# Performance work log

Hardware: AMD Instinct MI355X
Metric: run time of the kernel (lower is better)

The kernel has to match this reference:

```python
import jax, jax.numpy as jnp
import numpy as np

B, T, I, H, O = 8192, 1024, 2, 10, 2


def _gru_scan(gates_x, W_hh, b_hh, collect):
    """gates_x: [B,T,3H] precomputed input-side gates. Returns outputs [B,T,H] if collect else final h [B,H]."""
    def step(h, gx):
        gh = h @ W_hh.T + b_hh                      # [B,3H]
        xr, xz, xn = jnp.split(gx, 3, axis=-1)
        hr, hz, hn = jnp.split(gh, 3, axis=-1)
        r = jax.nn.sigmoid(xr + hr)
        z = jax.nn.sigmoid(xz + hz)
        n = jnp.tanh(xn + r * hn)
        h_new = (1.0 - z) * n + z * h
        return h_new, (h_new if collect else None)
    h0 = jnp.zeros((gates_x.shape[0], W_hh.shape[1]), gates_x.dtype)
    hT, ys = jax.lax.scan(step, h0, jnp.swapaxes(gates_x, 0, 1))  # scan over time
    return jnp.swapaxes(ys, 0, 1) if collect else hT


def setup_inputs() -> dict:
    key = jax.random.key(0)
    ks = jax.random.split(key, 12)
    s = 1.0 / np.sqrt(H)  # PyTorch GRU/Linear init scale
    u = lambda k, shp: jax.random.uniform(k, shp, jnp.float32, -s, s)
    return {
        "batchX": jax.random.normal(ks[0], (B, T, I), jnp.float32),
        "W_ih0": u(ks[1], (3 * H, I)),  "W_hh0": u(ks[2], (3 * H, H)),
        "b_ih0": u(ks[3], (3 * H,)),    "b_hh0": u(ks[4], (3 * H,)),
        "W_ih1": u(ks[5], (3 * H, H)),  "W_hh1": u(ks[6], (3 * H, H)),
        "b_ih1": u(ks[7], (3 * H,)),    "b_hh1": u(ks[8], (3 * H,)),
        "W_fc": u(ks[9], (O, H)),       "b_fc": u(ks[10], (O,)),
    }


def reference(batchX, W_ih0, W_hh0, b_ih0, b_hh0, W_ih1, W_hh1, b_ih1, b_hh1, W_fc, b_fc):
    # Layer 0: need full sequence of hidden states (feeds layer 1)
    gx0 = batchX @ W_ih0.T + b_ih0                  # [B,T,3H] one big GEMM
    h1 = _gru_scan(gx0, W_hh0, b_hh0, collect=True)  # [B,T,H]
    # Layer 1: only final hidden state is used by the head
    gx1 = h1 @ W_ih1.T + b_ih1                      # [B,T,3H]
    hT = _gru_scan(gx1, W_hh1, b_hh1, collect=False)  # [B,H]
    return hT @ W_fc.T + b_fc                       # [B,O]
```

## Files before the change

### kernel.cpp

```cpp
#include <hip/hip_runtime.h>

#define NB 8192
#define NT 1024
#define NH 10
#define ROWS_PER_WAVE 4
#define ROWS_PER_BLOCK 16

typedef float v2f __attribute__((ext_vector_type(2)));
typedef float v4f __attribute__((ext_vector_type(4)));

#define LOG2E 1.44269504088896340736f

__device__ __forceinline__ float rcpf(float x) { return __builtin_amdgcn_rcpf(x); }
__device__ __forceinline__ float exp2i(float x) {
#if __has_builtin(__builtin_amdgcn_exp2f)
    return __builtin_amdgcn_exp2f(x);
#else
    float r;
    asm("v_exp_f32 %0, %1" : "=v"(r) : "v"(x));
    return r;
#endif
}
__device__ __forceinline__ float tanh2u(float u) { return fmaf(-2.0f, rcpf(exp2i(u) + 1.0f), 1.0f); }
__device__ __forceinline__ void sigm2q2(float qa, float qb, float& sa, float& sb) {
    const float da = 1.0f + exp2i(qa);
    const float db = 1.0f + exp2i(qb);
    const float R = rcpf(da * db);
    sa = db * R;
    sb = da * R;
}

__device__ __forceinline__ v2f lo2(v4f a) { return __builtin_shufflevector(a, a, 0, 1); }
__device__ __forceinline__ v2f hi2(v4f a) { return __builtin_shufflevector(a, a, 2, 3); }
__device__ __forceinline__ v2f pkfma(v2f a, v2f b, v2f c) {
    return __builtin_elementwise_fma(a, b, c);
}

struct W5 { v2f p[5]; };
__device__ __forceinline__ W5 loadrow_scaled(const float* __restrict__ q, float s) {
    W5 w;
#pragma unroll
    for (int k = 0; k < 5; ++k) w.p[k] = (v2f){q[2 * k] * s, q[2 * k + 1] * s};
    return w;
}
__device__ __forceinline__ v2f dotWacc(const W5& w, v4f ha, v4f hb, v2f hc, v2f acc) {
    acc = pkfma(w.p[0], lo2(ha), acc);
    acc = pkfma(w.p[1], hi2(ha), acc);
    acc = pkfma(w.p[2], lo2(hb), acc);
    acc = pkfma(w.p[3], hi2(hb), acc);
    acc = pkfma(w.p[4], hc, acc);
    return acc;
}
__device__ __forceinline__ float hsum(v2f a) { return a.x + a.y; }

__global__ __launch_bounds__(256) void gru_fused(
    const float* __restrict__ X,
    const float* __restrict__ Wih0, const float* __restrict__ Whh0,
    const float* __restrict__ bih0, const float* __restrict__ bhh0,
    const float* __restrict__ Wih1, const float* __restrict__ Whh1,
    const float* __restrict__ bih1, const float* __restrict__ bhh1,
    const float* __restrict__ Wfc,  const float* __restrict__ bfc,
    float* __restrict__ out)
{
    __shared__ __align__(16) float hls[4][2][5][12];

    const int tid  = threadIdx.x;
    const int lane = tid & 63;
    const int wave = tid >> 6;
    const int g    = lane / 10;
    const int j    = lane - g * 10;
    const int gg   = (g < 4) ? g : 4;

    const bool active = (g < ROWS_PER_WAVE);
    int b = blockIdx.x * ROWS_PER_BLOCK + wave * ROWS_PER_WAVE + (active ? g : 0);
    const bool store_ok = active && (b < NB);
    if (b >= NB) b = NB - 1;

    const int r0 = j, r1 = j + 10, r2 = j + 20;
    const float Sz = -LOG2E;
    const float Sn = 2.0f * LOG2E;

    const v2f wxr = (v2f){Wih0[r0 * 2] * Sz, Wih0[r0 * 2 + 1] * Sz};
    const v2f wxz = (v2f){Wih0[r1 * 2] * Sz, Wih0[r1 * 2 + 1] * Sz};
    const v2f wxn = (v2f){Wih0[r2 * 2] * Sn, Wih0[r2 * 2 + 1] * Sn};

    const W5 whr0 = loadrow_scaled(Whh0 + r0 * NH, Sz);
    const W5 whz0 = loadrow_scaled(Whh0 + r1 * NH, Sz);
    const W5 whn0 = loadrow_scaled(Whh0 + r2 * NH, Sn);
    const W5 wir1 = loadrow_scaled(Wih1 + r0 * NH, Sz);
    const W5 wiz1 = loadrow_scaled(Wih1 + r1 * NH, Sz);
    const W5 win1 = loadrow_scaled(Wih1 + r2 * NH, Sn);
    const W5 whr1 = loadrow_scaled(Whh1 + r0 * NH, Sz);
    const W5 whz1 = loadrow_scaled(Whh1 + r1 * NH, Sz);
    const W5 whn1 = loadrow_scaled(Whh1 + r2 * NH, Sn);

    const v2f sr0 = (v2f){(bih0[r0] + bhh0[r0]) * Sz, 0.0f};
    const v2f sz0 = (v2f){(bih0[r1] + bhh0[r1]) * Sz, 0.0f};
    const v2f sx0 = (v2f){bih0[r2] * Sn, 0.0f};
    const v2f sh0 = (v2f){bhh0[r2] * Sn, 0.0f};
    const v2f sr1 = (v2f){(bih1[r0] + bhh1[r0]) * Sz, 0.0f};
    const v2f sz1 = (v2f){(bih1[r1] + bhh1[r1]) * Sz, 0.0f};
    const v2f sx1 = (v2f){bih1[r2] * Sn, 0.0f};
    const v2f sh1 = (v2f){bhh1[r2] * Sn, 0.0f};

    float* const L0 = &hls[wave][0][gg][0];
    float* const L1 = &hls[wave][1][gg][0];

    v4f h0a = (v4f){0,0,0,0}, h0b = (v4f){0,0,0,0}; v2f h0c = (v2f){0,0};
    v4f h1a, h1b; v2f h1c;
    v4f nh1a = (v4f){0,0,0,0}, nh1b = (v4f){0,0,0,0}; v2f nh1c = (v2f){0,0};
    float my0 = 0.0f, my1 = 0.0f;

    const float2* xp = reinterpret_cast<const float2*>(X) + (size_t)b * NT;
    float2 xc = xp[0];
    float2 xn2;

    v2f accr, accz, accx, acch, aqr, aqz, aqx, aqh;
    v4f nh0a, nh0b; v2f nh0c;
    float r0v, z0v, n0v, r1v, z1v, n1v;

#define L0_GATES(xv)                                                            \
    accr = pkfma(wxr, xv, sr0);                                                 \
    accz = pkfma(wxz, xv, sz0);                                                 \
    accx = pkfma(wxn, xv, sx0);                                                 \
    accr = dotWacc(whr0, h0a, h0b, h0c, accr);                                  \
    accz = dotWacc(whz0, h0a, h0b, h0c, accz);                                  \
    acch = dotWacc(whn0, h0a, h0b, h0c, sh0);                                   \
    sigm2q2(hsum(accr), hsum(accz), r0v, z0v);                                  \
    n0v = tanh2u(fmaf(r0v, hsum(acch), hsum(accx)));                            \
    my0 = fmaf(z0v, my0 - n0v, n0v);                                            \
    L0[j] = my0;                                                                \
    nh0a = *reinterpret_cast<const v4f*>(L0);                                   \
    nh0b = *reinterpret_cast<const v4f*>(L0 + 4);                               \
    nh0c = *reinterpret_cast<const v2f*>(L0 + 8)

#define L1_GATES()                                                              \
    aqr = dotWacc(whr1, h1a, h1b, h1c, sr1);                                    \
    aqz = dotWacc(whz1, h1a, h1b, h1c, sz1);                                    \
    aqh = dotWacc(whn1, h1a, h1b, h1c, sh1);                                    \
    aqr = dotWacc(wir1, h0a, h0b, h0c, aqr);                                    \
    aqz = dotWacc(wiz1, h0a, h0b, h0c, aqz);                                    \
    aqx = dotWacc(win1, h0a, h0b, h0c, sx1);                                    \
    sigm2q2(hsum(aqr), hsum(aqz), r1v, z1v);                                    \
    n1v = tanh2u(fmaf(r1v, hsum(aqh), hsum(aqx)));                              \
    my1 = fmaf(z1v, my1 - n1v, n1v)

    {
        const v2f xv = (v2f){xc.x, xc.y};
        L0_GATES(xv);
        h0a = nh0a; h0b = nh0b; h0c = nh0c;
        xc = xp[1];
    }

    for (int t = 1; t < NT; ++t) {
        xn2 = xp[(t + 1 < NT) ? (t + 1) : (NT - 1)];
        const v2f xv = (v2f){xc.x, xc.y};
        L0_GATES(xv);
        h1a = nh1a; h1b = nh1b; h1c = nh1c;
        L1_GATES();
        h0a = nh0a; h0b = nh0b; h0c = nh0c;
        L1[j] = my1;
        nh1a = *reinterpret_cast<const v4f*>(L1);
        nh1b = *reinterpret_cast<const v4f*>(L1 + 4);
        nh1c = *reinterpret_cast<const v2f*>(L1 + 8);
        xc = xn2;
    }

    {
        h1a = nh1a; h1b = nh1b; h1c = nh1c;
        L1_GATES();
        L1[j] = my1;
        h1a = *reinterpret_cast<const v4f*>(L1);
        h1b = *reinterpret_cast<const v4f*>(L1 + 4);
        h1c = *reinterpret_cast<const v2f*>(L1 + 8);
    }
#undef L0_GATES
#undef L1_GATES

    if (store_ok && j < 2) {
        const W5 wf = loadrow_scaled(Wfc + j * NH, 1.0f);
        out[(size_t)b * 2 + j] = hsum(dotWacc(wf, h1a, h1b, h1c, (v2f){bfc[j], 0.0f}));
    }
}

extern "C" void kernel_launch(void* const* d_in, const int* in_sizes, int n_in,
                              void* d_out, int out_size, void* d_ws, size_t ws_size,
                              hipStream_t stream) {
    const float* X    = (const float*)d_in[0];
    const float* Wih0 = (const float*)d_in[1];
    const float* Whh0 = (const float*)d_in[2];
    const float* bih0 = (const float*)d_in[3];
    const float* bhh0 = (const float*)d_in[4];
    const float* Wih1 = (const float*)d_in[5];
    const float* Whh1 = (const float*)d_in[6];
    const float* bih1 = (const float*)d_in[7];
    const float* bhh1 = (const float*)d_in[8];
    const float* Wfc  = (const float*)d_in[9];
    const float* bfc  = (const float*)d_in[10];
    float* out = (float*)d_out;

    const int grid = NB / ROWS_PER_BLOCK;
    gru_fused<<<grid, 256, 0, stream>>>(X, Wih0, Whh0, bih0, bhh0,
                                        Wih1, Whh1, bih1, bhh1, Wfc, bfc, out);
}
```

Before: 414.3 us.

## Software-pipeline GRU loop so layer-0 dots overlap layer-1 activation chain

Splits each layer's step into a dot-product phase and an activation/LDS-exchange phase, then rotates the loop so the layer-0 dot products for the next timestep are issued after the layer-1 work of the current one. The aim is to shorten the serial dependency chain per iteration and give the scheduler independent work to hide transcendental and LDS latency. The prologue and epilogue are restructured to match, which adds some code size and more live registers.

```diff
diff --git a/kernel.cpp b/kernel.cpp
--- a/kernel.cpp
+++ b/kernel.cpp
@@ -112,20 +112,13 @@
     float my0 = 0.0f, my1 = 0.0f;
 
     const float2* xp = reinterpret_cast<const float2*>(X) + (size_t)b * NT;
-    float2 xc = xp[0];
-    float2 xn2;
 
     v2f accr, accz, accx, acch, aqr, aqz, aqx, aqh;
     v4f nh0a, nh0b; v2f nh0c;
     float r0v, z0v, n0v, r1v, z1v, n1v;
-
-#define L0_GATES(xv)                                                            \
-    accr = pkfma(wxr, xv, sr0);                                                 \
-    accz = pkfma(wxz, xv, sz0);                                                 \
-    accx = pkfma(wxn, xv, sx0);                                                 \
-    accr = dotWacc(whr0, h0a, h0b, h0c, accr);                                  \
-    accz = dotWacc(whz0, h0a, h0b, h0c, accz);                                  \
-    acch = dotWacc(whn0, h0a, h0b, h0c, sh0);                                   \
+    float2 xc, xn2;
+
+#define L0_FINAL()                                                              \
     sigm2q2(hsum(accr), hsum(accz), r0v, z0v);                                  \
     n0v = tanh2u(fmaf(r0v, hsum(acch), hsum(accx)));                            \
     my0 = fmaf(z0v, my0 - n0v, n0v);                                            \
@@ -134,48 +127,75 @@
     nh0b = *reinterpret_cast<const v4f*>(L0 + 4);                               \
     nh0c = *reinterpret_cast<const v2f*>(L0 + 8)
 
-#define L1_GATES()                                                              \
+#define L0_DOTS(xv)                                                             \
+    accr = pkfma(wxr, xv, sr0);                                                 \
+    accz = pkfma(wxz, xv, sz0);                                                 \
+    accx = pkfma(wxn, xv, sx0);                                                 \
+    accr = dotWacc(whr0, h0a, h0b, h0c, accr);                                  \
+    accz = dotWacc(whz0, h0a, h0b, h0c, accz);                                  \
+    acch = dotWacc(whn0, h0a, h0b, h0c, sh0)
+
+#define L1_DOTS()                                                               \
     aqr = dotWacc(whr1, h1a, h1b, h1c, sr1);                                    \
     aqz = dotWacc(whz1, h1a, h1b, h1c, sz1);                                    \
     aqh = dotWacc(whn1, h1a, h1b, h1c, sh1);                                    \
     aqr = dotWacc(wir1, h0a, h0b, h0c, aqr);                                    \
     aqz = dotWacc(wiz1, h0a, h0b, h0c, aqz);                                    \
-    aqx = dotWacc(win1, h0a, h0b, h0c, sx1);                                    \
+    aqx = dotWacc(win1, h0a, h0b, h0c, sx1)
+
+#define L1_FINAL()                                                              \
     sigm2q2(hsum(aqr), hsum(aqz), r1v, z1v);                                    \
     n1v = tanh2u(fmaf(r1v, hsum(aqh), hsum(aqx)));                              \
-    my1 = fmaf(z1v, my1 - n1v, n1v)
+    my1 = fmaf(z1v, my1 - n1v, n1v);                                            \
+    L1[j] = my1;                                                                \
+    nh1a = *reinterpret_cast<const v4f*>(L1);                                   \
+    nh1b = *reinterpret_cast<const v4f*>(L1 + 4);                               \
+    nh1c = *reinterpret_cast<const v2f*>(L1 + 8)
 
     {
+        xc = xp[0];
+        const v2f xv0 = (v2f){xc.x, xc.y};
+        accr = pkfma(wxr, xv0, sr0);
+        accz = pkfma(wxz, xv0, sz0);
+        accx = pkfma(wxn, xv0, sx0);
+        acch = sh0;
+        xc = xp[1];
+        L0_FINAL();
+        h0a = nh0a; h0b = nh0b; h0c = nh0c;
+        const v2f xv1 = (v2f){xc.x, xc.y};
+        L0_DOTS(xv1);
+        xc = xp[2];
+    }
+
+    for (int i = 1; i <= NT - 2; ++i) {
+        xn2 = xp[(i + 2 <= NT - 1) ? (i + 2) : (NT - 1)];
+        L0_FINAL();
+        h1a = nh1a; h1b = nh1b; h1c = nh1c;
+        L1_DOTS();
+        L1_FINAL();
+        h0a = nh0a; h0b = nh0b; h0c = nh0c;
         const v2f xv = (v2f){xc.x, xc.y};
-        L0_GATES(xv);
+        L0_DOTS(xv);
+        xc = xn2;
+    }
+
+    {
+        L0_FINAL();
+        h1a = nh1a; h1b = nh1b; h1c = nh1c;
+        L1_DOTS();
+        L1_FINAL();
         h0a = nh0a; h0b = nh0b; h0c = nh0c;
-        xc = xp[1];
-    }
-
-    for (int t = 1; t < NT; ++t) {
-        xn2 = xp[(t + 1 < NT) ? (t + 1) : (NT - 1)];
-        const v2f xv = (v2f){xc.x, xc.y};
-        L0_GATES(xv);
-        h1a = nh1a; h1b = nh1b; h1c = nh1c;
-        L1_GATES();
-        h0a = nh0a; h0b = nh0b; h0c = nh0c;
-        L1[j] = my1;
-        nh1a = *reinterpret_cast<const v4f*>(L1);
-        nh1b = *reinterpret_cast<const v4f*>(L1 + 4);
-        nh1c = *reinterpret_cast<const v2f*>(L1 + 8);
-        xc = xn2;
-    }
-
+    }
     {
         h1a = nh1a; h1b = nh1b; h1c = nh1c;
-        L1_GATES();
-        L1[j] = my1;
-        h1a = *reinterpret_cast<const v4f*>(L1);
-        h1b = *reinterpret_cast<const v4f*>(L1 + 4);
-        h1c = *reinterpret_cast<const v2f*>(L1 + 8);
-    }
-#undef L0_GATES
-#undef L1_GATES
+        L1_DOTS();
+        L1_FINAL();
+        h1a = nh1a; h1b = nh1b; h1c = nh1c;
+    }
+#undef L0_FINAL
+#undef L0_DOTS
+#undef L1_DOTS
+#undef L1_FINAL
 
     if (store_ok && j < 2) {
         const W5 wf = loadrow_scaled(Wfc + j * NH, 1.0f);
```

Result: no change. 419.2 us (+1.2%).
